# Kernel optimization log

Hardware: AMD Instinct MI355X
Metric: run time of the kernel (lower is better)

The kernel has to match this reference:

```python
import jax, jax.numpy as jnp
import numpy as np

# SS2D (VMamba) dims
B, H, W, C = 2, 48, 48, 96
D_INNER, D_STATE, DT_RANK, K = 192, 32, 6, 4


def _silu(x):
    return x * jax.nn.sigmoid(x)


def setup_inputs() -> dict:
    key = jax.random.key(0)
    ks = jax.random.split(key, 8)
    inputs = jax.random.normal(ks[0], (B, H, W, C), jnp.float32)
    in_proj_w = jax.random.normal(ks[1], (2 * D_INNER, C), jnp.float32) * 0.02
    conv_w = jax.random.normal(ks[2], (D_INNER, 1, 3, 3), jnp.float32) * 0.1
    conv_b = jnp.zeros((D_INNER,), jnp.float32)
    x_proj_w = jax.random.normal(ks[3], (K, DT_RANK + 2 * D_STATE, D_INNER), jnp.float32) * 0.02
    dt_projs_w = jax.random.normal(ks[4], (K, D_INNER, DT_RANK), jnp.float32) * 0.1
    dt_projs_b = jax.random.uniform(ks[5], (K, D_INNER), jnp.float32, -4.0, -2.0)
    # S4D-real init: A_log[n] = log(n+1), tiled over K*d_inner
    A_logs = jnp.log(jnp.tile(jnp.arange(1, D_STATE + 1, dtype=jnp.float32), (K * D_INNER, 1)))
    Ds = jnp.ones((K * D_INNER,), jnp.float32)
    ln_w = jnp.ones((D_INNER,), jnp.float32)
    ln_b = jnp.zeros((D_INNER,), jnp.float32)
    out_proj_w = jax.random.normal(ks[6], (C, D_INNER), jnp.float32) * 0.02
    return dict(inputs=inputs, in_proj_w=in_proj_w, conv_w=conv_w, conv_b=conv_b,
                x_proj_w=x_proj_w, dt_projs_w=dt_projs_w, dt_projs_b=dt_projs_b,
                A_logs=A_logs, Ds=Ds, ln_w=ln_w, ln_b=ln_b, out_proj_w=out_proj_w)


def _selective_scan(us, deltas, A, Bs, Cs, Ds_kd):
    # us, deltas: (B,K,d,L); Bs, Cs: (B,K,N,L); A: (K,d,N); Ds_kd: (K,d)
    u_l = jnp.moveaxis(us, -1, 0)      # (L,B,K,d)
    d_l = jnp.moveaxis(deltas, -1, 0)  # (L,B,K,d)
    B_l = jnp.moveaxis(Bs, -1, 0)      # (L,B,K,N)
    C_l = jnp.moveaxis(Cs, -1, 0)      # (L,B,K,N)
    h0 = jnp.zeros(us.shape[:3] + (A.shape[-1],), us.dtype)  # (B,K,d,N)

    def step(h, inp):
        u, d, b, c = inp
        dA = jnp.exp(d[..., None] * A)                    # (B,K,d,N)
        h = h * dA + (d * u)[..., None] * b[:, :, None, :]
        y = jnp.einsum('bkdn,bkn->bkd', h, c)
        return h, y

    _, ys = jax.lax.scan(step, h0, (u_l, d_l, B_l, C_l))
    ys = jnp.moveaxis(ys, 0, -1)  # (B,K,d,L)
    return ys + Ds_kd[None, :, :, None] * us


def _ss2d(x, in_proj_w, conv_w, conv_b, x_proj_w, dt_projs_w, dt_projs_b,
          A_logs, Ds, ln_w, ln_b, out_proj_w):
    b, h, w, c = x.shape
    L = h * w
    xz = jnp.einsum('bhwc,ec->bhwe', x, in_proj_w)          # (B,H,W,2*d_inner)
    x_, z = jnp.split(xz, 2, axis=-1)
    # depthwise 3x3 conv (NCHW), SAME padding
    x_ = jnp.transpose(x_, (0, 3, 1, 2))                    # (B,d,H,W)
    x_ = jax.lax.conv_general_dilated(x_, conv_w, (1, 1), 'SAME',
                                      feature_group_count=D_INNER,
                                      dimension_numbers=('NCHW', 'OIHW', 'NCHW'))
    x_ = _silu(x_ + conv_b[None, :, None, None])
    # 4-direction scan inputs
    x_hw = x_.reshape(b, D_INNER, L)
    x_wh = jnp.transpose(x_, (0, 1, 3, 2)).reshape(b, D_INNER, L)
    xs = jnp.stack([x_hw, x_wh], axis=1)                    # (B,2,d,L)
    xs = jnp.concatenate([xs, jnp.flip(xs, axis=-1)], axis=1)  # (B,4,d,L)
    x_dbl = jnp.einsum('bkdl,kcd->bkcl', xs, x_proj_w)      # (B,4,dt_rank+2N,L)
    dts = x_dbl[:, :, :DT_RANK]
    Bs = x_dbl[:, :, DT_RANK:DT_RANK + D_STATE]
    Cs = x_dbl[:, :, DT_RANK + D_STATE:]
    dts = jnp.einsum('bkrl,kdr->bkdl', dts, dt_projs_w)
    deltas = jax.nn.softplus(dts + dt_projs_b[None, :, :, None])
    A = -jnp.exp(A_logs).reshape(K, D_INNER, D_STATE)
    Ds_kd = Ds.reshape(K, D_INNER)
    out_y = _selective_scan(xs, deltas, A, Bs, Cs, Ds_kd)   # (B,4,d,L)
    inv_y = jnp.flip(out_y[:, 2:4], axis=-1)                # (B,2,d,L)
    wh_y = jnp.transpose(out_y[:, 1].reshape(b, D_INNER, w, h), (0, 1, 3, 2)).reshape(b, D_INNER, L)
    invwh_y = jnp.transpose(inv_y[:, 1].reshape(b, D_INNER, w, h), (0, 1, 3, 2)).reshape(b, D_INNER, L)
    y = out_y[:, 0] + inv_y[:, 0] + wh_y + invwh_y          # (B,d,L)
    y = jnp.transpose(y, (0, 2, 1)).reshape(b, h, w, D_INNER)
    # LayerNorm over channel dim
    mu = jnp.mean(y, axis=-1, keepdims=True)
    var = jnp.var(y, axis=-1, keepdims=True)
    y = (y - mu) * jax.lax.rsqrt(var + 1e-5) * ln_w + ln_b
    y = y * _silu(z)
    return jnp.einsum('bhwd,cd->bhwc', y, out_proj_w)


def reference(inputs, in_proj_w, conv_w, conv_b, x_proj_w, dt_projs_w, dt_projs_b,
              A_logs, Ds, ln_w, ln_b, out_proj_w):
    attn = _ss2d(inputs, in_proj_w, conv_w, conv_b, x_proj_w, dt_projs_w,
                 dt_projs_b, A_logs, Ds, ln_w, ln_b, out_proj_w)
    return inputs + attn
```

## Files before the change

### kernel.cpp

```cpp
#include <hip/hip_runtime.h>
#include <math.h>

#define B_ 2
#define H_ 48
#define W_ 48
#define C_ 96
#define D_ 192
#define L_ 2304
#define K_ 4
#define NS 32
#define RK 6
#define CD 70

#define NC 16
#define CL (L_/NC)
#define NCH (B_*K_*D_)
#define LOG2E 1.44269504088896f

__device__ __forceinline__ float fexp2(float x) {
#if __has_builtin(__builtin_amdgcn_exp2f)
    return __builtin_amdgcn_exp2f(x);
#else
    return __expf(x * 0.69314718055994531f);
#endif
}

#define BDL (B_*D_*L_)
#define OFF_Z      0
#define OFF_XPRE   (OFF_Z    + BDL)
#define OFF_XHW    (OFF_XPRE + BDL)
#define OFF_XWH    (OFF_XHW  + BDL)
#define OFF_DELTA  (OFF_XWH  + BDL)
#define OFF_BS     (OFF_DELTA+ B_*K_*D_*L_)
#define OFF_CS     (OFF_BS   + B_*K_*L_*NS)
#define OFF_YS     (OFF_CS   + B_*K_*L_*NS)
#define OFF_YF     (OFF_YS   + B_*K_*L_*D_)

#define OFF_H0     OFF_YF

__global__ __launch_bounds__(256) void k1_inproj(const float* __restrict__ x,
        const float* __restrict__ w, float* __restrict__ ws) {
    __shared__ __align__(16) float Xs[24*128];
    int blk = blockIdx.x;
    int b = blk / 288;
    int rem = blk % 288;
    int l0 = (rem >> 2) * 32;
    int es = rem & 3;
    int tid = threadIdx.x;
    const float4* xs4 = (const float4*)(x + (size_t)(b*L_ + l0)*C_);
    #pragma unroll
    for (int it = 0; it < 3; ++it) {
        int i4 = it*256 + tid;
        float4 v = xs4[i4];
        int idx4 = i4*4;
        int p = idx4 / 96, c = idx4 % 96;
        *(float4*)&Xs[(c>>2)*128 + p*4] = v;
    }
    __syncthreads();
    int l = tid & 31, eg = tid >> 5;
    int pos = l0 + l;
    float acc[12];
    #pragma unroll
    for (int i = 0; i < 12; ++i) acc[i] = 0.f;
    const float4* wp[12];
    #pragma unroll
    for (int i = 0; i < 12; ++i) {
        int e = es*96 + eg*12 + i;
        wp[i] = (const float4*)(w + (size_t)e*96);
    }
    for (int q = 0; q < 24; ++q) {
        float4 xr = *(const float4*)&Xs[q*128 + l*4];
        #pragma unroll
        for (int i = 0; i < 12; ++i) {
            float4 wv = wp[i][q];
            acc[i] += xr.x*wv.x + xr.y*wv.y + xr.z*wv.z + xr.w*wv.w;
        }
    }
    if (es < 2) {
        float* xpre = ws + OFF_XPRE;
        #pragma unroll
        for (int i = 0; i < 12; ++i) {
            int e = es*96 + eg*12 + i;
            xpre[(size_t)(b*D_ + e)*L_ + pos] = acc[i];
        }
    } else {
        float* zp = ws + OFF_Z + (size_t)(b*L_ + pos)*D_ + (es-2)*96 + eg*12;
        #pragma unroll
        for (int q = 0; q < 3; ++q)
            *(float4*)&zp[q*4] = make_float4(acc[q*4], acc[q*4+1], acc[q*4+2], acc[q*4+3]);
    }
}

__global__ __launch_bounds__(256) void k2_conv(const float* __restrict__ cw,
        const float* __restrict__ cb, float* __restrict__ ws) {
    __shared__ float img[26*48];
    __shared__ float res[24*49];
    int blk = blockIdx.x;
    int bd = blk >> 1;
    int half = blk & 1;
    int d = bd % D_;
    int hh0 = half * 24;
    int tid = threadIdx.x;
    const float* xp = ws + OFF_XPRE + (size_t)bd*L_;
    for (int it = 0; it < 5; ++it) {
        int idx = it*256 + tid;
        if (idx < 26*48) {
            int gr = hh0 - 1 + idx/48;
            img[idx] = (gr >= 0 && gr < H_) ? xp[gr*48 + idx%48] : 0.f;
        }
    }
    float wr[9];
    #pragma unroll
    for (int j = 0; j < 9; ++j) wr[j] = cw[d*9 + j];
    float bias = cb[d];
    __syncthreads();
    float* hw = ws + OFF_XHW + (size_t)bd*L_ + hh0*48;
    for (int it = 0; it < 5; ++it) {
        int idx = it*256 + tid;
        if (idx < 24*48) {
            int r = idx/48, w0 = idx%48;
            float acc = bias;
            #pragma unroll
            for (int kh = 0; kh < 3; ++kh) {
                #pragma unroll
                for (int kw = 0; kw < 3; ++kw) {
                    int iw = w0 + kw - 1;
                    if (iw >= 0 && iw < W_)
                        acc = fmaf(img[(r+kh)*48 + iw], wr[kh*3 + kw], acc);
                }
            }
            float v = acc / (1.f + __expf(-acc));
            hw[idx] = v;
            res[r*49 + w0] = v;
        }
    }
    __syncthreads();
    float* wh = ws + OFF_XWH + (size_t)bd*L_;
    for (int it = 0; it < 5; ++it) {
        int idx = it*256 + tid;
        if (idx < 24*48) {
            int w0 = idx/24, r = idx%24;
            wh[w0*48 + hh0 + r] = res[r*49 + w0];
        }
    }
}

__global__ __launch_bounds__(256) void k3_xproj(const float* __restrict__ xpw,
        const float* __restrict__ dtw, const float* __restrict__ dtb,
        float* __restrict__ ws) {
    __shared__ __align__(16) float Xs[48*64];
    __shared__ float xd[CD*17];
    int blk = blockIdx.x;
    int b = blk / 576;
    int rem = blk % 576;
    int k = rem / 144;
    int l0 = (rem % 144) * 16;
    int tid = threadIdx.x;
    const float* src = ws + ((k & 1) ? OFF_XWH : OFF_XHW);
    bool flip = (k >= 2);
    #pragma unroll
    for (int it = 0; it < 12; ++it) {
        int idx = it*256 + tid;
        int d = idx >> 4, l = idx & 15;
        int pos = flip ? (L_ - 1 - (l0 + l)) : (l0 + l);
        Xs[(d>>2)*64 + l*4 + (d&3)] = src[(size_t)(b*D_ + d)*L_ + pos];
    }
    __syncthreads();
    int l = tid & 15, cg = tid >> 4;
    {
        float acc[5] = {0.f, 0.f, 0.f, 0.f, 0.f};
        const float4* wp[5];
        #pragma unroll
        for (int i = 0; i < 5; ++i) {
            int c = cg + 16*i;
            if (c >= CD) c = 0;
            wp[i] = (const float4*)(xpw + ((size_t)k*CD + c)*D_);
        }
        for (int q = 0; q < 48; ++q) {
            float4 xr = *(const float4*)&Xs[q*64 + l*4];
            #pragma unroll
            for (int i = 0; i < 5; ++i) {
                float4 wv = wp[i][q];
                acc[i] += xr.x*wv.x + xr.y*wv.y + xr.z*wv.z + xr.w*wv.w;
            }
        }
        #pragma unroll
        for (int i = 0; i < 5; ++i) {
            int c = cg + 16*i;
            if (c < CD) xd[c*17 + l] = acc[i];
        }
    }
    __syncthreads();
    {
        float r[6];
        #pragma unroll
        for (int rr = 0; rr < 6; ++rr) r[rr] = xd[rr*17 + l];
        float* dout = ws + OFF_DELTA + (size_t)(b*K_ + k)*D_*L_;
        int dg = tid >> 4;
        for (int i = 0; i < 12; ++i) {
            int d = dg*12 + i;
            const float* wdt = dtw + ((size_t)k*D_ + d)*6;
            float acc = dtb[k*D_ + d];
            #pragma unroll
            for (int rr = 0; rr < 6; ++rr) acc = fmaf(r[rr], wdt[rr], acc);
            float sp = fmaxf(acc, 0.f) + log1pf(__expf(-fabsf(acc)));
            dout[(size_t)d*L_ + l0 + l] = sp;
        }
    }
    {
        float* Bsp = ws + OFF_BS + ((size_t)(b*K_ + k)*L_ + l0)*NS;
        float* Csp = ws + OFF_CS + ((size_t)(b*K_ + k)*L_ + l0)*NS;
        int n = tid & 31, lq = tid >> 5;
        #pragma unroll
        for (int j = 0; j < 2; ++j) {
            int ll = lq + 8*j;
            Bsp[(size_t)ll*NS + n] = xd[(RK + n)*17 + ll];
            Csp[(size_t)ll*NS + n] = xd[(RK + NS + n)*17 + ll];
        }
    }
}

__global__ __launch_bounds__(512) void k4a_local(const float* __restrict__ Alogs,
        float* __restrict__ ws) {
    __shared__ float Pl[NC][NS];
    __shared__ float Hl[NC][NS];
    int blk = blockIdx.x;
    int d = blk % D_;
    int bk = blk / D_;
    int b = bk >> 2, k = bk & 3;
    int c = threadIdx.x >> 5;
    int n = threadIdx.x & 31;
    float a2 = -__expf(Alogs[((size_t)k*D_ + d)*NS + n]) * LOG2E;
    const float* dptr = ws + OFF_DELTA + (size_t)(bk*D_ + d)*L_ + c*CL;
    const float* ubase = ws + ((k & 1) ? OFF_XWH : OFF_XHW) + (size_t)(b*D_ + d)*L_;
    const float* Bsp = ws + OFF_BS + ((size_t)bk*L_ + c*CL)*NS;
    bool flip = (k >= 2);
    float h = 0.f, sd = 0.f;
    for (int lb = 0; lb < CL; lb += 4) {
        float4 d4 = *(const float4*)(dptr + lb);
        float4 t4;
        if (!flip) {
            t4 = *(const float4*)(ubase + c*CL + lb);
        } else {
            float4 r = *(const float4*)(ubase + (L_ - 4) - (c*CL + lb));
            t4 = make_float4(r.w, r.z, r.y, r.x);
        }
        float dl[4] = {d4.x, d4.y, d4.z, d4.w};
        float uu[4] = {t4.x, t4.y, t4.z, t4.w};
        #pragma unroll
        for (int j = 0; j < 4; ++j) {
            float bn = Bsp[(lb + j)*NS + n];
            float e = fexp2(dl[j]*a2);
            h = fmaf(h, e, dl[j]*uu[j]*bn);
            sd += dl[j];
        }
    }
    Pl[c][n] = fexp2(a2*sd);
    Hl[c][n] = h;
    __syncthreads();
    if (threadIdx.x < NS) {
        float hh = 0.f;
        #pragma unroll
        for (int cc = 0; cc < NC; ++cc) {
            float p  = Pl[cc][n];
            float hf = Hl[cc][n];
            Pl[cc][n] = hh;
            hh = fmaf(hh, p, hf);
        }
    }
    __syncthreads();
    ws[OFF_H0 + (size_t)(bk*D_ + d)*NC*NS + threadIdx.x] = Pl[c][n];
}

__global__ __launch_bounds__(512) void k4c_scan(const float* __restrict__ Alogs,
        const float* __restrict__ Dsp, float* __restrict__ ws) {
    __shared__ float yld[CL*17];
    int blk = blockIdx.x;
    int dg = blk % 12;
    int c  = (blk / 12) % NC;
    int bk = blk / (12*NC);
    int b = bk >> 2, k = bk & 3;
    int sw = threadIdx.x >> 5;
    int n  = threadIdx.x & 31;
    int d = dg*16 + sw;
    float a2 = -__expf(Alogs[((size_t)k*D_ + d)*NS + n]) * LOG2E;
    float dc = Dsp[k*D_ + d];
    const float* dptr = ws + OFF_DELTA + (size_t)(bk*D_ + d)*L_ + c*CL;
    const float* ubase = ws + ((k & 1) ? OFF_XWH : OFF_XHW) + (size_t)(b*D_ + d)*L_;
    const float* Bsp = ws + OFF_BS + ((size_t)bk*L_ + c*CL)*NS;
    const float* Csp = ws + OFF_CS + ((size_t)bk*L_ + c*CL)*NS;
    bool flip = (k >= 2);
    float h = ws[OFF_H0 + (size_t)(bk*D_ + d)*NC*NS + c*NS + n];
    int g = n >> 3;
    int off = ((g & 1) << 1) | (g >> 1);
    for (int lb = 0; lb < CL; lb += 4) {
        float4 d4 = *(const float4*)(dptr + lb);
        float4 t4;
        if (!flip) {
            t4 = *(const float4*)(ubase + c*CL + lb);
        } else {
            float4 r = *(const float4*)(ubase + (L_ - 4) - (c*CL + lb));
            t4 = make_float4(r.w, r.z, r.y, r.x);
        }
        float dl[4] = {d4.x, d4.y, d4.z, d4.w};
        float uu[4] = {t4.x, t4.y, t4.z, t4.w};
        float y[4];
        #pragma unroll
        for (int j = 0; j < 4; ++j) {
            float bn = Bsp[(lb + j)*NS + n];
            float cn = Csp[(lb + j)*NS + n];
            float e = fexp2(dl[j]*a2);
            h = fmaf(h, e, dl[j]*uu[j]*bn);
            y[j] = h * cn;
        }
        #pragma unroll
        for (int j = 0; j < 4; ++j) y[j] += __shfl_xor(y[j], 16);
        float z0 = (n & 16) ? y[1] : y[0];
        float z1 = (n & 16) ? y[3] : y[2];
        z0 += __shfl_xor(z0, 8);
        z1 += __shfl_xor(z1, 8);
        float wv = (n & 8) ? z1 : z0;
        wv += __shfl_xor(wv, 4);
        wv += __shfl_xor(wv, 2);
        wv += __shfl_xor(wv, 1);
        float ua = (n & 16) ? uu[1] : uu[0];
        float ub = (n & 16) ? uu[3] : uu[2];
        float us = (n & 8) ? ub : ua;
        if ((n & 7) == 0) yld[(lb + off)*17 + sw] = fmaf(dc, us, wv);
    }
    __syncthreads();
    float* ysp = ws + OFF_YS + ((size_t)bk*L_ + c*CL)*D_ + dg*16;
    for (int it = 0; it < 5; ++it) {
        int idx = it*512 + threadIdx.x;
        if (idx < CL*16) {
            int l = idx >> 4, dd = idx & 15;
            ysp[(size_t)l*D_ + dd] = yld[l*17 + dd];
        }
    }
}

__global__ __launch_bounds__(192) void k5_combine(const float* __restrict__ lnw,
        const float* __restrict__ lnb, float* __restrict__ ws) {
    int bp = blockIdx.x;
    int b = bp / L_, pos = bp % L_;
    int d = threadIdx.x;
    int hh = pos / W_, w0 = pos % W_;
    int poswh = w0*H_ + hh;
    const float* ys = ws + OFF_YS + (size_t)b*K_*L_*D_;
    float y = ys[(size_t)(0*L_ + pos)*D_ + d]
            + ys[(size_t)(2*L_ + (L_ - 1 - pos))*D_ + d]
            + ys[(size_t)(1*L_ + poswh)*D_ + d]
            + ys[(size_t)(3*L_ + (L_ - 1 - poswh))*D_ + d];
    float s = y, ss = y*y;
    #pragma unroll
    for (int m = 32; m >= 1; m >>= 1) {
        s  += __shfl_xor(s, m);
        ss += __shfl_xor(ss, m);
    }
    __shared__ float red[2][4];
    int wv = threadIdx.x >> 6;
    if ((threadIdx.x & 63) == 0) { red[0][wv] = s; red[1][wv] = ss; }
    __syncthreads();
    float su = red[0][0] + red[0][1] + red[0][2];
    float sq = red[1][0] + red[1][1] + red[1][2];
    float mu  = su * (1.f/192.f);
    float var = sq * (1.f/192.f) - mu*mu;
    float rs  = rsqrtf(var + 1e-5f);
    float yn = (y - mu)*rs*lnw[d] + lnb[d];
    float zv = ws[OFF_Z + (size_t)(b*L_ + pos)*D_ + d];
    float sz = zv / (1.f + __expf(-zv));
    ws[OFF_YF + (size_t)(b*L_ + pos)*D_ + d] = yn * sz;
}

__global__ __launch_bounds__(256) void k6_outproj(const float* __restrict__ w,
        const float* __restrict__ xin, float* __restrict__ out,
        const float* __restrict__ ws) {
    __shared__ __align__(16) float Ys[48*64];
    __shared__ float outT[16*49];
    int blk = blockIdx.x;
    int b = blk / 288;
    int rem = blk % 288;
    int l0 = (rem >> 1) * 16;
    int es = rem & 1;
    int tid = threadIdx.x;
    const float4* yf4 = (const float4*)(ws + OFF_YF + (size_t)(b*L_ + l0)*D_);
    #pragma unroll
    for (int it = 0; it < 3; ++it) {
        int i4 = it*256 + tid;
        float4 v = yf4[i4];
        int idx4 = i4*4;
        int p = idx4 / 192, dd = idx4 % 192;
        *(float4*)&Ys[(dd>>2)*64 + p*4] = v;
    }
    __syncthreads();
    int l = tid & 15, cg = tid >> 4;
    float acc[3] = {0.f, 0.f, 0.f};
    const float4* wp[3];
    #pragma unroll
    for (int i = 0; i < 3; ++i) {
        int c = es*48 + cg*3 + i;
        wp[i] = (const float4*)(w + (size_t)c*D_);
    }
    for (int q = 0; q < 48; ++q) {
        float4 xr = *(const float4*)&Ys[q*64 + l*4];
        #pragma unroll
        for (int i = 0; i < 3; ++i) {
            float4 wv = wp[i][q];
            acc[i] += xr.x*wv.x + xr.y*wv.y + xr.z*wv.z + xr.w*wv.w;
        }
    }
    #pragma unroll
    for (int i = 0; i < 3; ++i) outT[l*49 + cg*3 + i] = acc[i];
    __syncthreads();
    #pragma unroll
    for (int it = 0; it < 3; ++it) {
        int idx = it*256 + tid;
        int p = idx / 48, cc = idx % 48;
        size_t o = (size_t)(b*L_ + l0 + p)*C_ + es*48 + cc;
        out[o] = xin[o] + outT[p*49 + cc];
    }
}

extern "C" void kernel_launch(void* const* d_in, const int* in_sizes, int n_in,
                              void* d_out, int out_size, void* d_ws, size_t ws_size,
                              hipStream_t stream) {
    const float* x        = (const float*)d_in[0];
    const float* in_proj  = (const float*)d_in[1];
    const float* conv_w   = (const float*)d_in[2];
    const float* conv_b   = (const float*)d_in[3];
    const float* x_proj_w = (const float*)d_in[4];
    const float* dt_w     = (const float*)d_in[5];
    const float* dt_b     = (const float*)d_in[6];
    const float* A_logs   = (const float*)d_in[7];
    const float* Ds       = (const float*)d_in[8];
    const float* ln_w     = (const float*)d_in[9];
    const float* ln_b     = (const float*)d_in[10];
    const float* out_w    = (const float*)d_in[11];
    float* out = (float*)d_out;
    float* ws  = (float*)d_ws;

    k1_inproj <<<576,  256, 0, stream>>>(x, in_proj, ws);
    k2_conv   <<<768,  256, 0, stream>>>(conv_w, conv_b, ws);
    k3_xproj  <<<1152, 256, 0, stream>>>(x_proj_w, dt_w, dt_b, ws);
    k4a_local <<<NCH,  512, 0, stream>>>(A_logs, ws);
    k4c_scan  <<<1536, 512, 0, stream>>>(A_logs, Ds, ws);
    k5_combine<<<B_*L_,192, 0, stream>>>(ln_w, ln_b, ws);
    k6_outproj<<<576,  256, 0, stream>>>(out_w, x, out, ws);
}
```

Baseline: 289.5 us.

## Transpose B/C layout to per-state rows and fuse combine with output projection

The x-projection kernel now writes B and C as [n][L] instead of [L][n], so the scan kernels can load four timesteps per state with one float4 instead of scalar strided loads. The D*u skip term is folded into each lane's partial sum as D/32*u before the warp reduction, which removes the select logic after it. The LayerNorm/gating combine kernel and the output projection are merged into one kernel that handles 16 positions and all 96 output channels, removing the YF round trip and one launch. The fused kernel has only 288 blocks, which may leave the GPU underoccupied.

```diff
diff --git a/kernel.cpp b/kernel.cpp
--- a/kernel.cpp
+++ b/kernel.cpp
@@ -208,14 +208,14 @@
         }
     }
     {
-        float* Bsp = ws + OFF_BS + ((size_t)(b*K_ + k)*L_ + l0)*NS;
-        float* Csp = ws + OFF_CS + ((size_t)(b*K_ + k)*L_ + l0)*NS;
-        int n = tid & 31, lq = tid >> 5;
+        float* Bb = ws + OFF_BS + (size_t)(b*K_ + k)*NS*L_;
+        float* Cb = ws + OFF_CS + (size_t)(b*K_ + k)*NS*L_;
+        int ll = tid & 15, nh = tid >> 4;
         #pragma unroll
         for (int j = 0; j < 2; ++j) {
-            int ll = lq + 8*j;
-            Bsp[(size_t)ll*NS + n] = xd[(RK + n)*17 + ll];
-            Csp[(size_t)ll*NS + n] = xd[(RK + NS + n)*17 + ll];
+            int n = nh + 16*j;
+            Bb[(size_t)n*L_ + l0 + ll] = xd[(RK + n)*17 + ll];
+            Cb[(size_t)n*L_ + l0 + ll] = xd[(RK + NS + n)*17 + ll];
         }
     }
 }
@@ -233,11 +233,12 @@
     float a2 = -__expf(Alogs[((size_t)k*D_ + d)*NS + n]) * LOG2E;
     const float* dptr = ws + OFF_DELTA + (size_t)(bk*D_ + d)*L_ + c*CL;
     const float* ubase = ws + ((k & 1) ? OFF_XWH : OFF_XHW) + (size_t)(b*D_ + d)*L_;
-    const float* Bsp = ws + OFF_BS + ((size_t)bk*L_ + c*CL)*NS;
+    const float* Bp = ws + OFF_BS + ((size_t)bk*NS + n)*L_ + c*CL;
     bool flip = (k >= 2);
     float h = 0.f, sd = 0.f;
     for (int lb = 0; lb < CL; lb += 4) {
         float4 d4 = *(const float4*)(dptr + lb);
+        float4 b4 = *(const float4*)(Bp + lb);
         float4 t4;
         if (!flip) {
             t4 = *(const float4*)(ubase + c*CL + lb);
@@ -247,11 +248,11 @@
         }
         float dl[4] = {d4.x, d4.y, d4.z, d4.w};
         float uu[4] = {t4.x, t4.y, t4.z, t4.w};
+        float bb[4] = {b4.x, b4.y, b4.z, b4.w};
         #pragma unroll
         for (int j = 0; j < 4; ++j) {
-            float bn = Bsp[(lb + j)*NS + n];
             float e = fexp2(dl[j]*a2);
-            h = fmaf(h, e, dl[j]*uu[j]*bn);
+            h = fmaf(h, e, dl[j]*uu[j]*bb[j]);
             sd += dl[j];
         }
     }
@@ -284,17 +285,19 @@
     int n  = threadIdx.x & 31;
     int d = dg*16 + sw;
     float a2 = -__expf(Alogs[((size_t)k*D_ + d)*NS + n]) * LOG2E;
-    float dc = Dsp[k*D_ + d];
+    float dc32 = Dsp[k*D_ + d] * (1.f/32.f);
     const float* dptr = ws + OFF_DELTA + (size_t)(bk*D_ + d)*L_ + c*CL;
     const float* ubase = ws + ((k & 1) ? OFF_XWH : OFF_XHW) + (size_t)(b*D_ + d)*L_;
-    const float* Bsp = ws + OFF_BS + ((size_t)bk*L_ + c*CL)*NS;
-    const float* Csp = ws + OFF_CS + ((size_t)bk*L_ + c*CL)*NS;
+    const float* Bp = ws + OFF_BS + ((size_t)bk*NS + n)*L_ + c*CL;
+    const float* Cp = ws + OFF_CS + ((size_t)bk*NS + n)*L_ + c*CL;
     bool flip = (k >= 2);
     float h = ws[OFF_H0 + (size_t)(bk*D_ + d)*NC*NS + c*NS + n];
     int g = n >> 3;
     int off = ((g & 1) << 1) | (g >> 1);
     for (int lb = 0; lb < CL; lb += 4) {
         float4 d4 = *(const float4*)(dptr + lb);
+        float4 b4 = *(const float4*)(Bp + lb);
+        float4 c4 = *(const float4*)(Cp + lb);
         float4 t4;
         if (!flip) {
             t4 = *(const float4*)(ubase + c*CL + lb);
@@ -304,14 +307,14 @@
         }
         float dl[4] = {d4.x, d4.y, d4.z, d4.w};
         float uu[4] = {t4.x, t4.y, t4.z, t4.w};
+        float bb[4] = {b4.x, b4.y, b4.z, b4.w};
+        float cc[4] = {c4.x, c4.y, c4.z, c4.w};
         float y[4];
         #pragma unroll
         for (int j = 0; j < 4; ++j) {
-            float bn = Bsp[(lb + j)*NS + n];
-            float cn = Csp[(lb + j)*NS + n];
             float e = fexp2(dl[j]*a2);
-            h = fmaf(h, e, dl[j]*uu[j]*bn);
-            y[j] = h * cn;
+            h = fmaf(h, e, dl[j]*uu[j]*bb[j]);
+            y[j] = fmaf(h, cc[j], dc32*uu[j]);
         }
         #pragma unroll
         for (int j = 0; j < 4; ++j) y[j] += __shfl_xor(y[j], 16);
@@ -323,10 +326,7 @@
         wv += __shfl_xor(wv, 4);
         wv += __shfl_xor(wv, 2);
         wv += __shfl_xor(wv, 1);
-        float ua = (n & 16) ? uu[1] : uu[0];
-        float ub = (n & 16) ? uu[3] : uu[2];
-        float us = (n & 8) ? ub : ua;
-        if ((n & 7) == 0) yld[(lb + off)*17 + sw] = fmaf(dc, us, wv);
+        if ((n & 7) == 0) yld[(lb + off)*17 + sw] = wv;
     }
     __syncthreads();
     float* ysp = ws + OFF_YS + ((size_t)bk*L_ + c*CL)*D_ + dg*16;
@@ -339,85 +339,94 @@
     }
 }
 
-__global__ __launch_bounds__(192) void k5_combine(const float* __restrict__ lnw,
-        const float* __restrict__ lnb, float* __restrict__ ws) {
-    int bp = blockIdx.x;
-    int b = bp / L_, pos = bp % L_;
-    int d = threadIdx.x;
-    int hh = pos / W_, w0 = pos % W_;
-    int poswh = w0*H_ + hh;
-    const float* ys = ws + OFF_YS + (size_t)b*K_*L_*D_;
-    float y = ys[(size_t)(0*L_ + pos)*D_ + d]
-            + ys[(size_t)(2*L_ + (L_ - 1 - pos))*D_ + d]
-            + ys[(size_t)(1*L_ + poswh)*D_ + d]
-            + ys[(size_t)(3*L_ + (L_ - 1 - poswh))*D_ + d];
-    float s = y, ss = y*y;
-    #pragma unroll
-    for (int m = 32; m >= 1; m >>= 1) {
-        s  += __shfl_xor(s, m);
-        ss += __shfl_xor(ss, m);
-    }
-    __shared__ float red[2][4];
-    int wv = threadIdx.x >> 6;
-    if ((threadIdx.x & 63) == 0) { red[0][wv] = s; red[1][wv] = ss; }
-    __syncthreads();
-    float su = red[0][0] + red[0][1] + red[0][2];
-    float sq = red[1][0] + red[1][1] + red[1][2];
-    float mu  = su * (1.f/192.f);
-    float var = sq * (1.f/192.f) - mu*mu;
-    float rs  = rsqrtf(var + 1e-5f);
-    float yn = (y - mu)*rs*lnw[d] + lnb[d];
-    float zv = ws[OFF_Z + (size_t)(b*L_ + pos)*D_ + d];
-    float sz = zv / (1.f + __expf(-zv));
-    ws[OFF_YF + (size_t)(b*L_ + pos)*D_ + d] = yn * sz;
-}
-
-__global__ __launch_bounds__(256) void k6_outproj(const float* __restrict__ w,
+__global__ __launch_bounds__(256) void k56_fused(const float* __restrict__ lnw,
+        const float* __restrict__ lnb, const float* __restrict__ w,
         const float* __restrict__ xin, float* __restrict__ out,
         const float* __restrict__ ws) {
-    __shared__ __align__(16) float Ys[48*64];
-    __shared__ float outT[16*49];
-    int blk = blockIdx.x;
-    int b = blk / 288;
-    int rem = blk % 288;
-    int l0 = (rem >> 1) * 16;
-    int es = rem & 1;
+    __shared__ __align__(16) float YsT[16*196];
+    __shared__ float psum[16][17], psq[16][17];
+    __shared__ float outT[16*97];
+    int blk = blockIdx.x;
+    int b = blk / 144;
+    int l0 = (blk % 144) * 16;
     int tid = threadIdx.x;
-    const float4* yf4 = (const float4*)(ws + OFF_YF + (size_t)(b*L_ + l0)*D_);
-    #pragma unroll
-    for (int it = 0; it < 3; ++it) {
-        int i4 = it*256 + tid;
-        float4 v = yf4[i4];
-        int idx4 = i4*4;
-        int p = idx4 / 192, dd = idx4 % 192;
-        *(float4*)&Ys[(dd>>2)*64 + p*4] = v;
-    }
-    __syncthreads();
-    int l = tid & 15, cg = tid >> 4;
-    float acc[3] = {0.f, 0.f, 0.f};
-    const float4* wp[3];
-    #pragma unroll
-    for (int i = 0; i < 3; ++i) {
-        int c = es*48 + cg*3 + i;
-        wp[i] = (const float4*)(w + (size_t)c*D_);
-    }
-    for (int q = 0; q < 48; ++q) {
-        float4 xr = *(const float4*)&Ys[q*64 + l*4];
-        #pragma unroll
-        for (int i = 0; i < 3; ++i) {
-            float4 wv = wp[i][q];
-            acc[i] += xr.x*wv.x + xr.y*wv.y + xr.z*wv.z + xr.w*wv.w;
-        }
-    }
-    #pragma unroll
-    for (int i = 0; i < 3; ++i) outT[l*49 + cg*3 + i] = acc[i];
-    __syncthreads();
-    #pragma unroll
-    for (int it = 0; it < 3; ++it) {
+    {
+        int p = tid >> 4, dg = tid & 15;
+        int pos = l0 + p;
+        int hh = pos / W_, w0 = pos % W_;
+        int poswh = w0*H_ + hh;
+        const float* ysb = ws + OFF_YS + (size_t)b*K_*L_*D_;
+        const float* r0 = ysb + (size_t)(0*L_ + pos)*D_;
+        const float* r1 = ysb + (size_t)(1*L_ + poswh)*D_;
+        const float* r2 = ysb + (size_t)(2*L_ + (L_-1-pos))*D_;
+        const float* r3 = ysb + (size_t)(3*L_ + (L_-1-poswh))*D_;
+        float yv[12];
+        float s = 0.f, sq = 0.f;
+        #pragma unroll
+        for (int i = 0; i < 12; i += 4) {
+            int d = dg*12 + i;
+            float4 v0 = *(const float4*)(r0 + d);
+            float4 v1 = *(const float4*)(r1 + d);
+            float4 v2 = *(const float4*)(r2 + d);
+            float4 v3 = *(const float4*)(r3 + d);
+            float y0 = v0.x+v1.x+v2.x+v3.x;
+            float y1 = v0.y+v1.y+v2.y+v3.y;
+            float y2 = v0.z+v1.z+v2.z+v3.z;
+            float y3 = v0.w+v1.w+v2.w+v3.w;
+            yv[i]=y0; yv[i+1]=y1; yv[i+2]=y2; yv[i+3]=y3;
+            s += y0+y1+y2+y3;
+            sq += y0*y0+y1*y1+y2*y2+y3*y3;
+        }
+        psum[p][dg] = s; psq[p][dg] = sq;
+        __syncthreads();
+        float su = 0.f, ssq = 0.f;
+        #pragma unroll
+        for (int j = 0; j < 16; ++j) { su += psum[p][j]; ssq += psq[p][j]; }
+        float mu  = su * (1.f/192.f);
+        float var = ssq * (1.f/192.f) - mu*mu;
+        float rs  = rsqrtf(var + 1e-5f);
+        const float* zp = ws + OFF_Z + (size_t)(b*L_ + pos)*D_;
+        #pragma unroll
+        for (int i = 0; i < 12; i += 4) {
+            int d = dg*12 + i;
+            float4 o;
+            float* oo = (float*)&o;
+            #pragma unroll
+            for (int jj = 0; jj < 4; ++jj) {
+                float yn = (yv[i+jj] - mu)*rs*lnw[d+jj] + lnb[d+jj];
+                float zv = zp[d+jj];
+                float sz = zv / (1.f + __expf(-zv));
+                oo[jj] = yn * sz;
+            }
+            *(float4*)&YsT[p*196 + d] = o;
+        }
+    }
+    __syncthreads();
+    {
+        int l = tid & 15, cg = tid >> 4;
+        float acc[6] = {0.f,0.f,0.f,0.f,0.f,0.f};
+        const float4* wp[6];
+        #pragma unroll
+        for (int i = 0; i < 6; ++i)
+            wp[i] = (const float4*)(w + (size_t)(cg*6 + i)*D_);
+        for (int q = 0; q < 48; ++q) {
+            float4 xr = *(const float4*)&YsT[l*196 + q*4];
+            #pragma unroll
+            for (int i = 0; i < 6; ++i) {
+                float4 wv = wp[i][q];
+                acc[i] += xr.x*wv.x + xr.y*wv.y + xr.z*wv.z + xr.w*wv.w;
+            }
+        }
+        #pragma unroll
+        for (int i = 0; i < 6; ++i) outT[l*97 + cg*6 + i] = acc[i];
+    }
+    __syncthreads();
+    #pragma unroll
+    for (int it = 0; it < 6; ++it) {
         int idx = it*256 + tid;
-        int p = idx / 48, cc = idx % 48;
-        size_t o = (size_t)(b*L_ + l0 + p)*C_ + es*48 + cc;
-        out[o] = xin[o] + outT[p*49 + cc];
+        int p = idx / 96, cc = idx % 96;
+        size_t o = (size_t)(b*L_ + l0 + p)*C_ + cc;
+        out[o] = xin[o] + outT[p*97 + cc];
     }
 }
 
@@ -444,6 +453,5 @@
     k3_xproj  <<<1152, 256, 0, stream>>>(x_proj_w, dt_w, dt_b, ws);
     k4a_local <<<NCH,  512, 0, stream>>>(A_logs, ws);
     k4c_scan  <<<1536, 512, 0, stream>>>(A_logs, Ds, ws);
-    k5_combine<<<B_*L_,192, 0, stream>>>(ln_w, ln_b, ws);
-    k6_outproj<<<576,  256, 0, stream>>>(out_w, x, out, ws);
-}
+    k56_fused <<<288,  256, 0, stream>>>(ln_w, ln_b, out_w, x, out, ws);
+}
```

Result: slower. 424.2 us (+46.5%).
